# Optimization experiments

Hardware: AMD Instinct MI355X
Metric: run time of the kernel (lower is better)

The kernel has to match this reference:

```python
import jax, jax.numpy as jnp
import numpy as np

N = 50000
E = 800000
D_IN = 128
H = 128
K = 64
BN_EPS = 1e-5


def setup_inputs() -> dict:
    key = jax.random.key(0)
    ks = jax.random.split(key, 16)
    s_in = 1.0 / np.sqrt(D_IN)
    s_h = 1.0 / np.sqrt(H)
    inp = {
        "x": jax.random.normal(ks[0], (N, D_IN), dtype=jnp.float32),
        "edge_index": jax.random.randint(ks[1], (2, E), 0, N, dtype=jnp.int64),
        # GIN layer 1 MLP (Linear(D_IN,H) -> ReLU -> Linear(H,H)), eps1, BN1
        "W1a": jax.random.uniform(ks[2], (D_IN, H), jnp.float32, -s_in, s_in),
        "b1a": jnp.zeros((H,), jnp.float32),
        "W1b": jax.random.uniform(ks[3], (H, H), jnp.float32, -s_h, s_h),
        "b1b": jnp.zeros((H,), jnp.float32),
        "eps1": jnp.zeros((), jnp.float32),
        "gamma1": jnp.ones((H,), jnp.float32),
        "beta1": jnp.zeros((H,), jnp.float32),
        # GIN layer 2 MLP, eps2, BN2
        "W2a": jax.random.uniform(ks[4], (H, H), jnp.float32, -s_h, s_h),
        "b2a": jnp.zeros((H,), jnp.float32),
        "W2b": jax.random.uniform(ks[5], (H, H), jnp.float32, -s_h, s_h),
        "b2b": jnp.zeros((H,), jnp.float32),
        "eps2": jnp.zeros((), jnp.float32),
        "gamma2": jnp.ones((H,), jnp.float32),
        "beta2": jnp.zeros((H,), jnp.float32),
        # final projection (no bias) and learnable log temperature
        "Wout": jax.random.uniform(ks[6], (H, K), jnp.float32, -s_h, s_h),
        "log_tau": jnp.zeros((), jnp.float32),  # log(1.0)
    }
    return inp


def _gin_layer(x, src, dst, Wa, ba, Wb, bb, eps):
    # GINConv: mlp((1+eps)*x + sum_{j in N(i)} x_j), scatter-add over edges
    agg = jax.ops.segment_sum(x[src], dst, num_segments=N)  # [N, d]
    h = (1.0 + eps) * x + agg
    h = jax.nn.relu(h @ Wa + ba) @ Wb + bb
    return h


def _batchnorm(x, gamma, beta):
    # training-mode BatchNorm1d over node dim (biased variance)
    m = jnp.mean(x, axis=0)
    v = jnp.mean(jnp.square(x - m), axis=0)
    return (x - m) * jax.lax.rsqrt(v + BN_EPS) * gamma + beta


def reference(x, edge_index, W1a, b1a, W1b, b1b, eps1, gamma1, beta1,
              W2a, b2a, W2b, b2b, eps2, gamma2, beta2, Wout, log_tau):
    src, dst = edge_index[0], edge_index[1]
    h = _gin_layer(x, src, dst, W1a, b1a, W1b, b1b, eps1)
    h = jax.nn.relu(_batchnorm(h, gamma1, beta1))
    h = _gin_layer(h, src, dst, W2a, b2a, W2b, b2b, eps2)
    h = jax.nn.relu(_batchnorm(h, gamma2, beta2))
    logits = h @ Wout  # [N, K]
    tau = jnp.exp(log_tau)
    S = jax.nn.softmax(logits / tau, axis=-1)
    return (S, logits)
```

## Files before the change

kernel.cpp:

```cpp
#include <hip/hip_runtime.h>
#include <hip/hip_fp16.h>


#define NNODES 50000
#define NEDGES 800000
#define HD 128
#define KOUT 64
#define NCLS 8
#define CLSW 6250
#define HIST_BLKS 512

typedef __attribute__((ext_vector_type(8))) _Float16 f16x8;
typedef __attribute__((ext_vector_type(4))) float f32x4;

__device__ __forceinline__ unsigned short f2h_bits(float f) {
    _Float16 h = (_Float16)f;
    return __builtin_bit_cast(unsigned short, h);
}
__device__ __forceinline__ f16x8 h8_relu(f16x8 v) {
    #pragma unroll
    for (int i = 0; i < 8; ++i) v[i] = (v[i] > (_Float16)0.f) ? v[i] : (_Float16)0.f;
    return v;
}

__global__ __launch_bounds__(256) void prep_all(
    const float* __restrict__ x, unsigned short* __restrict__ xh,
    const float* __restrict__ W1a, const float* __restrict__ W1b,
    const float* __restrict__ W2a, const float* __restrict__ W2b,
    unsigned short* __restrict__ wt1a, unsigned short* __restrict__ wt1b,
    unsigned short* __restrict__ wt2a, unsigned short* __restrict__ wt2b,
    const int* __restrict__ ei, int* __restrict__ deg)
{
    __shared__ int h[CLSW];
    int bid = blockIdx.x;
    if (bid < HIST_BLKS) {
        const int cls = bid & 7;
        const int lo = cls * CLSW;
        const int e0 = (bid >> 3) * 12500;
        for (int i = threadIdx.x; i < CLSW; i += 256) h[i] = 0;
        __syncthreads();
        for (int e = e0 + threadIdx.x; e < e0 + 12500; e += 256) {
            unsigned d = (unsigned)(ei[NEDGES + e] - lo);
            if (d < (unsigned)CLSW) atomicAdd(&h[d], 1);
        }
        __syncthreads();
        for (int i = threadIdx.x; i < CLSW; i += 256) {
            int v = h[i];
            if (v) atomicAdd(&deg[lo + i], v);
        }
    } else if (bid < HIST_BLKS + 6250) {
        int i = (bid - HIST_BLKS) * 256 + threadIdx.x;
        float4 v = ((const float4*)x)[i];
        ushort4 o;
        o.x = f2h_bits(v.x); o.y = f2h_bits(v.y);
        o.z = f2h_bits(v.z); o.w = f2h_bits(v.w);
        ((ushort4*)xh)[i] = o;
    } else {
        int wb = bid - (HIST_BLKS + 6250);
        int w = wb >> 6;
        int idx = (wb & 63) * 256 + threadIdx.x;
        int n = idx >> 7, k = idx & 127;
        const float* W = (w == 0) ? W1a : (w == 1) ? W1b : (w == 2) ? W2a : W2b;
        unsigned short* Wt = (w == 0) ? wt1a : (w == 1) ? wt1b : (w == 2) ? wt2a : wt2b;
        Wt[idx] = f2h_bits(W[k * HD + n]);
    }
}

__global__ __launch_bounds__(256) void scan_a(
    const int* __restrict__ deg, int* __restrict__ incl, int* __restrict__ bsum)
{
    __shared__ int s[256];
    int t = threadIdx.x, idx = blockIdx.x * 256 + t;
    int v = (idx < NNODES) ? deg[idx] : 0;
    s[t] = v; __syncthreads();
    #pragma unroll
    for (int off = 1; off < 256; off <<= 1) {
        int tmp = (t >= off) ? s[t - off] : 0;
        __syncthreads();
        s[t] += tmp;
        __syncthreads();
    }
    if (idx < NNODES) incl[idx] = s[t];
    if (t == 255) bsum[blockIdx.x] = s[255];
}

__global__ __launch_bounds__(256) void scan_c(
    const int* __restrict__ deg, const int* __restrict__ incl,
    const int* __restrict__ bsum,
    int* __restrict__ row_start, int* __restrict__ cur)
{
    __shared__ int s[256];
    int b = blockIdx.x, t = threadIdx.x;
    int p = 0;
    for (int i = t; i < b; i += 256) p += bsum[i];
    s[t] = p; __syncthreads();
    #pragma unroll
    for (int off = 128; off > 0; off >>= 1) {
        if (t < off) s[t] += s[t + off];
        __syncthreads();
    }
    int off0 = s[0];
    int idx = b * 256 + t;
    if (idx >= NNODES) return;
    int ex = incl[idx] - deg[idx] + off0;
    row_start[idx] = ex;
    cur[idx] = ex;
}

__global__ __launch_bounds__(256) void edge_fill(
    const int* __restrict__ ei, int* __restrict__ cur, int* __restrict__ col)
{
    const int cls = blockIdx.x & 7;
    const int e0 = (blockIdx.x >> 3) * 3125;
    for (int e = e0 + threadIdx.x; e < e0 + 3125; e += 256) {
        int dst = ei[NEDGES + e];
        if (dst / CLSW == cls) {
            int pos = atomicAdd(&cur[dst], 1);
            col[pos] = ei[e];
        }
    }
}

template<bool BN>
__global__ __launch_bounds__(256) void gin_gather_w(
    const unsigned short* __restrict__ Xh, const int* __restrict__ col,
    const int* __restrict__ rs, const int* __restrict__ re,
    const float* __restrict__ eps,
    const float* __restrict__ scale, const float* __restrict__ shift,
    unsigned short* __restrict__ H0h)
{
    const int t = threadIdx.x;
    const int g = t >> 4;
    const int lane = t & 15;
    const f16x8* X8 = (const f16x8*)Xh;
    const float alphaf = 1.f + eps[0];

    f16x8 sc8, sh8, al8;
    #pragma unroll
    for (int i = 0; i < 8; ++i) al8[i] = (_Float16)alphaf;
    if (BN) {
        #pragma unroll
        for (int i = 0; i < 8; ++i) {
            sc8[i] = (_Float16)scale[lane * 8 + i];
            sh8[i] = (_Float16)shift[lane * 8 + i];
        }
    }

    #pragma unroll 1
    for (int nn = 0; nn < 2; ++nn) {
        int node = blockIdx.x * 32 + nn * 16 + g;
        if (node >= NNODES) continue;

        f16x8 acc = X8[(long)node * 16 + lane];
        if (BN) acc = h8_relu(acc * sc8 + sh8);
        acc = acc * al8;

        int j = rs[node], end = re[node];
        for (; j + 7 < end; j += 8) {
            int c0 = col[j],     c1 = col[j + 1], c2 = col[j + 2], c3 = col[j + 3];
            int c4 = col[j + 4], c5 = col[j + 5], c6 = col[j + 6], c7 = col[j + 7];
            f16x8 u0 = X8[(long)c0 * 16 + lane];
            f16x8 u1 = X8[(long)c1 * 16 + lane];
            f16x8 u2 = X8[(long)c2 * 16 + lane];
            f16x8 u3 = X8[(long)c3 * 16 + lane];
            f16x8 u4 = X8[(long)c4 * 16 + lane];
            f16x8 u5 = X8[(long)c5 * 16 + lane];
            f16x8 u6 = X8[(long)c6 * 16 + lane];
            f16x8 u7 = X8[(long)c7 * 16 + lane];
            if (BN) {
                u0 = h8_relu(u0 * sc8 + sh8); u1 = h8_relu(u1 * sc8 + sh8);
                u2 = h8_relu(u2 * sc8 + sh8); u3 = h8_relu(u3 * sc8 + sh8);
                u4 = h8_relu(u4 * sc8 + sh8); u5 = h8_relu(u5 * sc8 + sh8);
                u6 = h8_relu(u6 * sc8 + sh8); u7 = h8_relu(u7 * sc8 + sh8);
            }
            acc += ((u0 + u1) + (u2 + u3)) + ((u4 + u5) + (u6 + u7));
        }
        for (; j + 3 < end; j += 4) {
            f16x8 u0 = X8[(long)col[j]     * 16 + lane];
            f16x8 u1 = X8[(long)col[j + 1] * 16 + lane];
            f16x8 u2 = X8[(long)col[j + 2] * 16 + lane];
            f16x8 u3 = X8[(long)col[j + 3] * 16 + lane];
            if (BN) {
                u0 = h8_relu(u0 * sc8 + sh8); u1 = h8_relu(u1 * sc8 + sh8);
                u2 = h8_relu(u2 * sc8 + sh8); u3 = h8_relu(u3 * sc8 + sh8);
            }
            acc += (u0 + u1) + (u2 + u3);
        }
        for (; j < end; ++j) {
            f16x8 u = X8[(long)col[j] * 16 + lane];
            if (BN) u = h8_relu(u * sc8 + sh8);
            acc += u;
        }

        ((f16x8*)H0h)[(long)node * 16 + lane] = acc;
    }
}

__global__ __launch_bounds__(512) void mlp_mfma(
    const unsigned short* __restrict__ A,
    const unsigned short* __restrict__ Wta,
    const float* __restrict__ biasa,
    const unsigned short* __restrict__ Wtb,
    const float* __restrict__ biasb,
    unsigned short* __restrict__ Cb,
    float* __restrict__ Cf,
    float* __restrict__ out_sum, float* __restrict__ out_sq)
{
    __shared__ float4 smem4[69632 / 16];
    char* smem = (char*)smem4;
    _Float16 (*Wsa)[136]  = (_Float16(*)[136])smem;
    _Float16 (*Wsb)[136]  = (_Float16(*)[136])(smem + 34816);
    _Float16 (*Cs16)[136] = (_Float16(*)[136])smem;
    float (*CsF)[132]     = (float(*)[132])smem;
    float* redp           = (float*)smem;

    const int t = threadIdx.x;
    const int wave = t >> 6, lane = t & 63;
    const int m16 = lane & 15, quad = lane >> 4;
    const int row0 = blockIdx.x * 128;
    const int arow = row0 + wave * 16 + m16;

    #pragma unroll
    for (int i = 0; i < 4; ++i) {
        int idx = t + i * 512;
        int r = idx >> 4, s = idx & 15;
        *(float4*)&Wsa[r][s * 8] = ((const float4*)Wta)[idx];
        *(float4*)&Wsb[r][s * 8] = ((const float4*)Wtb)[idx];
    }

    f16x8 afrag[4];
    if (arow < NNODES) {
        const _Float16* ar = (const _Float16*)A + (long)arow * HD + quad * 8;
        #pragma unroll
        for (int kc = 0; kc < 4; ++kc)
            afrag[kc] = *(const f16x8*)(ar + kc * 32);
    } else {
        #pragma unroll
        for (int kc = 0; kc < 4; ++kc)
            afrag[kc] = f16x8{0, 0, 0, 0, 0, 0, 0, 0};
    }
    __syncthreads();

    f32x4 accs[8];
    #pragma unroll
    for (int np = 0; np < 8; np += 2) {
        f32x4 a0 = {0.f, 0.f, 0.f, 0.f};
        f32x4 a1 = {0.f, 0.f, 0.f, 0.f};
        const _Float16* b0 = &Wsa[np * 16 + m16][quad * 8];
        const _Float16* b1 = &Wsa[(np + 1) * 16 + m16][quad * 8];
        #pragma unroll
        for (int kc = 0; kc < 4; ++kc) {
            f16x8 f0 = *(const f16x8*)(b0 + kc * 32);
            f16x8 f1 = *(const f16x8*)(b1 + kc * 32);
            a0 = __builtin_amdgcn_mfma_f32_16x16x32_f16(afrag[kc], f0, a0, 0, 0, 0);
            a1 = __builtin_amdgcn_mfma_f32_16x16x32_f16(afrag[kc], f1, a1, 0, 0, 0);
        }
        accs[np] = a0; accs[np + 1] = a1;
    }
    __syncthreads();

    #pragma unroll
    for (int np = 0; np < 8; ++np) {
        int c = np * 16 + m16;
        float bb = biasa[c];
        #pragma unroll
        for (int r = 0; r < 4; ++r)
            Cs16[wave * 16 + quad * 4 + r][c] =
                (_Float16)fmaxf(accs[np][r] + bb, 0.f);
    }
    __syncthreads();

    f16x8 afrag2[4];
    {
        const int crow = wave * 16 + m16;
        #pragma unroll
        for (int kc = 0; kc < 4; ++kc)
            afrag2[kc] = *(const f16x8*)&Cs16[crow][quad * 8 + kc * 32];
    }
    #pragma unroll
    for (int np = 0; np < 8; np += 2) {
        f32x4 a0 = {0.f, 0.f, 0.f, 0.f};
        f32x4 a1 = {0.f, 0.f, 0.f, 0.f};
        const _Float16* b0 = &Wsb[np * 16 + m16][quad * 8];
        const _Float16* b1 = &Wsb[(np + 1) * 16 + m16][quad * 8];
        #pragma unroll
        for (int kc = 0; kc < 4; ++kc) {
            f16x8 f0 = *(const f16x8*)(b0 + kc * 32);
            f16x8 f1 = *(const f16x8*)(b1 + kc * 32);
            a0 = __builtin_amdgcn_mfma_f32_16x16x32_f16(afrag2[kc], f0, a0, 0, 0, 0);
            a1 = __builtin_amdgcn_mfma_f32_16x16x32_f16(afrag2[kc], f1, a1, 0, 0, 0);
        }
        accs[np] = a0; accs[np + 1] = a1;
    }
    __syncthreads();

    #pragma unroll
    for (int np = 0; np < 8; ++np) {
        int c = np * 16 + m16;
        float bb = biasb[c];
        #pragma unroll
        for (int r = 0; r < 4; ++r)
            CsF[wave * 16 + quad * 4 + r][c] = accs[np][r] + bb;
    }
    __syncthreads();

    const int s4 = t & 31;
    const int rb = t >> 5;
    float lsum[4] = {}, lsq[4] = {};
    #pragma unroll
    for (int i = 0; i < 8; ++i) {
        int r = rb + i * 16;
        int row = row0 + r;
        float4 v = *(const float4*)&CsF[r][s4 * 4];
        if (row < NNODES) {
            if (Cb) {
                ushort4 o;
                o.x = f2h_bits(v.x); o.y = f2h_bits(v.y);
                o.z = f2h_bits(v.z); o.w = f2h_bits(v.w);
                ((ushort4*)Cb)[(long)row * 32 + s4] = o;
            }
            if (Cf) ((float4*)Cf)[(long)row * 32 + s4] = v;
            lsum[0] += v.x; lsum[1] += v.y; lsum[2] += v.z; lsum[3] += v.w;
            lsq[0] = fmaf(v.x, v.x, lsq[0]);
            lsq[1] = fmaf(v.y, v.y, lsq[1]);
            lsq[2] = fmaf(v.z, v.z, lsq[2]);
            lsq[3] = fmaf(v.w, v.w, lsq[3]);
        }
    }
    __syncthreads();

    #pragma unroll
    for (int j = 0; j < 4; ++j) {
        redp[(0 * 16 + rb) * 128 + s4 * 4 + j] = lsum[j];
        redp[(1 * 16 + rb) * 128 + s4 * 4 + j] = lsq[j];
    }
    __syncthreads();
    if (t < 128) {
        float s = 0.f, q = 0.f;
        #pragma unroll
        for (int g = 0; g < 16; ++g) {
            s += redp[g * 128 + t];
            q += redp[(16 + g) * 128 + t];
        }
        const int cls = blockIdx.x & 7;
        atomicAdd(&out_sum[cls * 128 + t], s);
        atomicAdd(&out_sq[cls * 128 + t],  q);
    }
}

__global__ void bn_prep(const float* __restrict__ ssum, const float* __restrict__ ssq,
                        const float* __restrict__ gamma, const float* __restrict__ beta,
                        float* __restrict__ scale, float* __restrict__ shift)
{
    int c = threadIdx.x;
    float s = 0.f, q = 0.f;
    #pragma unroll
    for (int g = 0; g < 8; ++g) {
        s += ssum[g * 128 + c];
        q += ssq[g * 128 + c];
    }
    const float invN = 1.0f / (float)NNODES;
    float m = s * invN;
    float var = fmaf(-m, m, q * invN);
    float rs = rsqrtf(var + 1e-5f);
    float sc = gamma[c] * rs;
    scale[c] = sc;
    shift[c] = beta[c] - m * sc;
}

__global__ __launch_bounds__(256) void out_proj_softmax(
    const float* __restrict__ H, const float* __restrict__ Wout,
    const float* __restrict__ scale, const float* __restrict__ shift,
    const float* __restrict__ log_tau,
    float* __restrict__ outS, float* __restrict__ outL)
{
    __shared__ float As[HD][20];
    const int t = threadIdx.x;
    const long row0 = (long)blockIdx.x * 16;

    #pragma unroll
    for (int i = 0; i < 8; ++i) {
        int idx = t + i * 256;
        int r = idx >> 7, cc = idx & 127;
        float v = H[(row0 + r) * HD + cc];
        As[cc][r] = fmaxf(fmaf(v, scale[cc], shift[cc]), 0.f);
    }
    __syncthreads();

    const int c = t & 63;
    const int g = t >> 6;
    float acc[4] = {};

    float wq[8];
    #pragma unroll
    for (int i = 0; i < 8; ++i) wq[i] = Wout[i * KOUT + c];

    #pragma unroll 1
    for (int kc = 0; kc < HD; kc += 8) {
        float wn[8];
        if (kc + 8 < HD) {
            #pragma unroll
            for (int i = 0; i < 8; ++i) wn[i] = Wout[(kc + 8 + i) * KOUT + c];
        }
        #pragma unroll
        for (int i = 0; i < 8; ++i) {
            float4 a = *(const float4*)&As[kc + i][g * 4];
            acc[0] = fmaf(a.x, wq[i], acc[0]);
            acc[1] = fmaf(a.y, wq[i], acc[1]);
            acc[2] = fmaf(a.z, wq[i], acc[2]);
            acc[3] = fmaf(a.w, wq[i], acc[3]);
        }
        if (kc + 8 < HD) {
            #pragma unroll
            for (int i = 0; i < 8; ++i) wq[i] = wn[i];
        }
    }

    float inv_tau = __expf(-log_tau[0]);
    #pragma unroll
    for (int i = 0; i < 4; ++i) {
        float z = acc[i] * inv_tau;
        float m = z;
        #pragma unroll
        for (int o = 32; o > 0; o >>= 1) m = fmaxf(m, __shfl_xor(m, o));
        float e = __expf(z - m);
        float s = e;
        #pragma unroll
        for (int o = 32; o > 0; o >>= 1) s += __shfl_xor(s, o);
        long oi = (row0 + g * 4 + i) * KOUT + c;
        outS[oi] = e / s;
        outL[oi] = acc[i];
    }
}

extern "C" void kernel_launch(void* const* d_in, const int* in_sizes, int n_in,
                              void* d_out, int out_size, void* d_ws, size_t ws_size,
                              hipStream_t stream)
{
    const float* x      = (const float*)d_in[0];
    const int*   ei     = (const int*)d_in[1];
    const float* W1a    = (const float*)d_in[2];
    const float* b1a    = (const float*)d_in[3];
    const float* W1b    = (const float*)d_in[4];
    const float* b1b    = (const float*)d_in[5];
    const float* eps1   = (const float*)d_in[6];
    const float* gamma1 = (const float*)d_in[7];
    const float* beta1  = (const float*)d_in[8];
    const float* W2a    = (const float*)d_in[9];
    const float* b2a    = (const float*)d_in[10];
    const float* W2b    = (const float*)d_in[11];
    const float* b2b    = (const float*)d_in[12];
    const float* eps2   = (const float*)d_in[13];
    const float* gamma2 = (const float*)d_in[14];
    const float* beta2  = (const float*)d_in[15];
    const float* Wout   = (const float*)d_in[16];
    const float* ltau   = (const float*)d_in[17];

    const size_t NB = (size_t)NNODES * HD;
    float* B0 = (float*)d_ws;
    float* B1 = B0 + NB;
    float* B2 = B1 + NB;
    float* ST = B2 + NB;
    float* sum1 = ST, *sq1 = ST + 1024, *sum2 = ST + 2048, *sq2 = ST + 3072;
    float* scale1 = ST + 4096, *shift1 = ST + 4224;
    float* scale2 = ST + 4352, *shift2 = ST + 4480;

    unsigned short* xh  = (unsigned short*)B2;
    unsigned short* h0h = (unsigned short*)B0;
    unsigned short* hh  = (unsigned short*)B0;
    unsigned short* h2h = (unsigned short*)B2;

    int* I0        = (int*)(ST + 4608);
    int* deg       = I0;
    int* incl      = I0 + 50048;
    int* row_start = I0 + 2 * 50048;
    int* cur       = I0 + 3 * 50048;
    int* bsum      = I0 + 4 * 50048;
    int* col       = bsum + 256;
    unsigned short* wt1a = (unsigned short*)(col + NEDGES);
    unsigned short* wt1b = wt1a + HD * HD;
    unsigned short* wt2a = wt1b + HD * HD;
    unsigned short* wt2b = wt2a + HD * HD;

    const int SCAN_BLKS = (NNODES + 255) / 256;
    const int GEMM_BLKS = (NNODES + 127) / 128;
    const int GATH_BLKS = (NNODES + 31) / 32;

    hipMemsetAsync(ST, 0, 4096 * sizeof(float), stream);
    hipMemsetAsync(deg, 0, NNODES * sizeof(int), stream);
    prep_all<<<HIST_BLKS + 6506, 256, 0, stream>>>(x, xh, W1a, W1b, W2a, W2b,
                                                   wt1a, wt1b, wt2a, wt2b, ei, deg);
    scan_a<<<SCAN_BLKS, 256, 0, stream>>>(deg, incl, bsum);
    scan_c<<<SCAN_BLKS, 256, 0, stream>>>(deg, incl, bsum, row_start, cur);
    edge_fill<<<2048, 256, 0, stream>>>(ei, cur, col);

    gin_gather_w<false><<<GATH_BLKS, 256, 0, stream>>>(
        xh, col, row_start, cur, eps1, nullptr, nullptr, h0h);
    mlp_mfma<<<GEMM_BLKS, 512, 0, stream>>>(
        h0h, wt1a, b1a, wt1b, b1b, hh, nullptr, sum1, sq1);
    bn_prep<<<1, 128, 0, stream>>>(sum1, sq1, gamma1, beta1, scale1, shift1);

    gin_gather_w<true><<<GATH_BLKS, 256, 0, stream>>>(
        hh, col, row_start, cur, eps2, scale1, shift1, h2h);
    mlp_mfma<<<GEMM_BLKS, 512, 0, stream>>>(
        h2h, wt2a, b2a, wt2b, b2b, nullptr, B1, sum2, sq2);
    bn_prep<<<1, 128, 0, stream>>>(sum2, sq2, gamma2, beta2, scale2, shift2);

    out_proj_softmax<<<NNODES / 16, 256, 0, stream>>>(
        B1, Wout, scale2, shift2, ltau,
        (float*)d_out, (float*)d_out + (size_t)NNODES * KOUT);
}
```

Before: 294.8 us.

## Fold BN prep into consumer kernels and store layer-2 MLP output as fp16

Removes the two single-block bn_prep launches. Each gather and output-projection block now recomputes the BN scale and shift from the partial sums into shared memory. The second MLP also writes fp16 instead of fp32, halving its output write and the out_proj read. The costs are redundant per-block BN folding plus an extra barrier, and reduced precision in the pre-BN activations fed to the final projection.

```diff
diff --git a/kernel.cpp b/kernel.cpp
--- a/kernel.cpp
+++ b/kernel.cpp
@@ -21,6 +21,25 @@
     #pragma unroll
     for (int i = 0; i < 8; ++i) v[i] = (v[i] > (_Float16)0.f) ? v[i] : (_Float16)0.f;
     return v;
+}
+__device__ __forceinline__ void bn_fold_ch(
+    const float* __restrict__ ssum, const float* __restrict__ ssq,
+    const float* __restrict__ gamma, const float* __restrict__ beta,
+    int c, float* sc_out, float* sh_out)
+{
+    float s = 0.f, q = 0.f;
+    #pragma unroll
+    for (int g = 0; g < 8; ++g) {
+        s += ssum[g * 128 + c];
+        q += ssq[g * 128 + c];
+    }
+    const float invN = 1.0f / (float)NNODES;
+    float m = s * invN;
+    float var = fmaf(-m, m, q * invN);
+    float rs = rsqrtf(var + 1e-5f);
+    float sc = gamma[c] * rs;
+    *sc_out = sc;
+    *sh_out = fmaf(-m, sc, beta[c]);
 }
 
 __global__ __launch_bounds__(256) void prep_all(
@@ -126,23 +145,30 @@
     const unsigned short* __restrict__ Xh, const int* __restrict__ col,
     const int* __restrict__ rs, const int* __restrict__ re,
     const float* __restrict__ eps,
-    const float* __restrict__ scale, const float* __restrict__ shift,
+    const float* __restrict__ ssum, const float* __restrict__ ssq,
+    const float* __restrict__ gamma, const float* __restrict__ beta,
     unsigned short* __restrict__ H0h)
 {
+    __shared__ float s_sc[128], s_sh[128];
     const int t = threadIdx.x;
     const int g = t >> 4;
     const int lane = t & 15;
     const f16x8* X8 = (const f16x8*)Xh;
     const float alphaf = 1.f + eps[0];
 
+    if (BN) {
+        if (t < 128) bn_fold_ch(ssum, ssq, gamma, beta, t, &s_sc[t], &s_sh[t]);
+        __syncthreads();
+    }
+
     f16x8 sc8, sh8, al8;
     #pragma unroll
     for (int i = 0; i < 8; ++i) al8[i] = (_Float16)alphaf;
     if (BN) {
         #pragma unroll
         for (int i = 0; i < 8; ++i) {
-            sc8[i] = (_Float16)scale[lane * 8 + i];
-            sh8[i] = (_Float16)shift[lane * 8 + i];
+            sc8[i] = (_Float16)s_sc[lane * 8 + i];
+            sh8[i] = (_Float16)s_sh[lane * 8 + i];
         }
     }
 
@@ -203,7 +229,6 @@
     const unsigned short* __restrict__ Wtb,
     const float* __restrict__ biasb,
     unsigned short* __restrict__ Cb,
-    float* __restrict__ Cf,
     float* __restrict__ out_sum, float* __restrict__ out_sq)
 {
     __shared__ float4 smem4[69632 / 16];
@@ -313,13 +338,10 @@
         int row = row0 + r;
         float4 v = *(const float4*)&CsF[r][s4 * 4];
         if (row < NNODES) {
-            if (Cb) {
-                ushort4 o;
-                o.x = f2h_bits(v.x); o.y = f2h_bits(v.y);
-                o.z = f2h_bits(v.z); o.w = f2h_bits(v.w);
-                ((ushort4*)Cb)[(long)row * 32 + s4] = o;
-            }
-            if (Cf) ((float4*)Cf)[(long)row * 32 + s4] = v;
+            ushort4 o;
+            o.x = f2h_bits(v.x); o.y = f2h_bits(v.y);
+            o.z = f2h_bits(v.z); o.w = f2h_bits(v.w);
+            ((ushort4*)Cb)[(long)row * 32 + s4] = o;
             lsum[0] += v.x; lsum[1] += v.y; lsum[2] += v.z; lsum[3] += v.w;
             lsq[0] = fmaf(v.x, v.x, lsq[0]);
             lsq[1] = fmaf(v.y, v.y, lsq[1]);
@@ -348,42 +370,30 @@
     }
 }
 
-__global__ void bn_prep(const float* __restrict__ ssum, const float* __restrict__ ssq,
-                        const float* __restrict__ gamma, const float* __restrict__ beta,
-                        float* __restrict__ scale, float* __restrict__ shift)
-{
-    int c = threadIdx.x;
-    float s = 0.f, q = 0.f;
-    #pragma unroll
-    for (int g = 0; g < 8; ++g) {
-        s += ssum[g * 128 + c];
-        q += ssq[g * 128 + c];
-    }
-    const float invN = 1.0f / (float)NNODES;
-    float m = s * invN;
-    float var = fmaf(-m, m, q * invN);
-    float rs = rsqrtf(var + 1e-5f);
-    float sc = gamma[c] * rs;
-    scale[c] = sc;
-    shift[c] = beta[c] - m * sc;
-}
-
 __global__ __launch_bounds__(256) void out_proj_softmax(
-    const float* __restrict__ H, const float* __restrict__ Wout,
-    const float* __restrict__ scale, const float* __restrict__ shift,
+    const unsigned short* __restrict__ Hh, const float* __restrict__ Wout,
+    const float* __restrict__ ssum, const float* __restrict__ ssq,
+    const float* __restrict__ gamma, const float* __restrict__ beta,
     const float* __restrict__ log_tau,
     float* __restrict__ outS, float* __restrict__ outL)
 {
     __shared__ float As[HD][20];
+    __shared__ float s_sc[128], s_sh[128];
     const int t = threadIdx.x;
     const long row0 = (long)blockIdx.x * 16;
 
-    #pragma unroll
-    for (int i = 0; i < 8; ++i) {
-        int idx = t + i * 256;
-        int r = idx >> 7, cc = idx & 127;
-        float v = H[(row0 + r) * HD + cc];
-        As[cc][r] = fmaxf(fmaf(v, scale[cc], shift[cc]), 0.f);
+    if (t < 128) bn_fold_ch(ssum, ssq, gamma, beta, t, &s_sc[t], &s_sh[t]);
+    __syncthreads();
+
+    {
+        int r = t >> 4;
+        int c0 = (t & 15) * 8;
+        f16x8 v8 = *(const f16x8*)(Hh + (row0 + r) * HD + c0);
+        #pragma unroll
+        for (int i = 0; i < 8; ++i) {
+            int cc = c0 + i;
+            As[cc][r] = fmaxf(fmaf((float)v8[i], s_sc[cc], s_sh[cc]), 0.f);
+        }
     }
     __syncthreads();
 
@@ -462,15 +472,14 @@
     float* B2 = B1 + NB;
     float* ST = B2 + NB;
     float* sum1 = ST, *sq1 = ST + 1024, *sum2 = ST + 2048, *sq2 = ST + 3072;
-    float* scale1 = ST + 4096, *shift1 = ST + 4224;
-    float* scale2 = ST + 4352, *shift2 = ST + 4480;
 
     unsigned short* xh  = (unsigned short*)B2;
     unsigned short* h0h = (unsigned short*)B0;
     unsigned short* hh  = (unsigned short*)B0;
     unsigned short* h2h = (unsigned short*)B2;
-
-    int* I0        = (int*)(ST + 4608);
+    unsigned short* B1h = (unsigned short*)B1;
+
+    int* I0        = (int*)(ST + 4096);
     int* deg       = I0;
     int* incl      = I0 + 50048;
     int* row_start = I0 + 2 * 50048;
@@ -495,18 +504,18 @@
     edge_fill<<<2048, 256, 0, stream>>>(ei, cur, col);
 
     gin_gather_w<false><<<GATH_BLKS, 256, 0, stream>>>(
-        xh, col, row_start, cur, eps1, nullptr, nullptr, h0h);
+        xh, col, row_start, cur, eps1,
+        nullptr, nullptr, nullptr, nullptr, h0h);
     mlp_mfma<<<GEMM_BLKS, 512, 0, stream>>>(
-        h0h, wt1a, b1a, wt1b, b1b, hh, nullptr, sum1, sq1);
-    bn_prep<<<1, 128, 0, stream>>>(sum1, sq1, gamma1, beta1, scale1, shift1);
+        h0h, wt1a, b1a, wt1b, b1b, hh, sum1, sq1);
 
     gin_gather_w<true><<<GATH_BLKS, 256, 0, stream>>>(
-        hh, col, row_start, cur, eps2, scale1, shift1, h2h);
+        hh, col, row_start, cur, eps2,
+        sum1, sq1, gamma1, beta1, h2h);
     mlp_mfma<<<GEMM_BLKS, 512, 0, stream>>>(
-        h2h, wt2a, b2a, wt2b, b2b, nullptr, B1, sum2, sq2);
-    bn_prep<<<1, 128, 0, stream>>>(sum2, sq2, gamma2, beta2, scale2, shift2);
+        h2h, wt2a, b2a, wt2b, b2b, B1h, sum2, sq2);
 
     out_proj_softmax<<<NNODES / 16, 256, 0, stream>>>(
-        B1, Wout, scale2, shift2, ltau,
+        B1h, Wout, sum2, sq2, gamma2, beta2, ltau,
         (float*)d_out, (float*)d_out + (size_t)NNODES * KOUT);
 }
```

After: 293.7 us. No clear change (-0.4%).
